# Performance work log

Hardware: AMD Instinct MI355X
Metric: run time of the kernel (lower is better)

Reference implementation:

```python
import jax, jax.numpy as jnp
import numpy as np

B, DIM, N = 4, 256, 2048
HEADS, DIM_HEAD = 8, 64
HIDDEN = HEADS * DIM_HEAD
SCALE = DIM_HEAD ** -0.5


def setup_inputs() -> dict:
    key = jax.random.key(0)
    k0, k1, k2, k3 = jax.random.split(key, 4)
    x = jax.random.normal(k0, (B, DIM, N), dtype=jnp.float32)
    # Conv1d kernel-size-1 weights == plain matrices over channels
    w_qkv = jax.random.normal(k1, (3 * HIDDEN, DIM), dtype=jnp.float32) * (DIM ** -0.5)
    w_out = jax.random.normal(k2, (DIM, HIDDEN), dtype=jnp.float32) * (HIDDEN ** -0.5)
    b_out = jax.random.normal(k3, (DIM,), dtype=jnp.float32) * 0.01
    return {"x": x, "w_qkv": w_qkv, "w_out": w_out, "b_out": b_out}


def reference(x, w_qkv, w_out, b_out):
    b, c, n = x.shape
    # 1x1 conv projection: [3H, C] x [b, C, n] -> [b, 3H, n]
    qkv = jnp.einsum('oc,bcn->bon', w_qkv, x)
    q, k, v = jnp.split(qkv, 3, axis=1)
    # [b, heads, dim_head, n]
    q = q.reshape(b, HEADS, DIM_HEAD, n) * SCALE
    k = k.reshape(b, HEADS, DIM_HEAD, n)
    v = v.reshape(b, HEADS, DIM_HEAD, n)
    sim = jnp.einsum('bhcn,bhcm->bhnm', q, k)          # [b,h,n,n]
    attn = jax.nn.softmax(sim, axis=-1)
    out = jnp.einsum('bhnm,bhcm->bhcn', attn, v)       # [b,h,dh,n]
    out = out.reshape(b, HIDDEN, n)
    return jnp.einsum('oc,bcn->bon', w_out, out) + b_out[None, :, None]
```

## Files before the change

### kernel.cpp

```cpp
#include <hip/hip_runtime.h>
#include <math.h>

#define BB 4
#define CDIM 256
#define NN 2048
#define HEADS 8
#define DH 64
#define HIDDEN 512
#define THREEH 1536
#define QSCALE 0.18033688011112042f

typedef __attribute__((ext_vector_type(8))) short bf16x8;
typedef __attribute__((ext_vector_type(4))) float f32x4;
typedef __attribute__((ext_vector_type(4))) unsigned uint4v;

static __device__ inline unsigned short f2bf(float f) {
    unsigned u = __float_as_uint(f);
    u += 0x7fff + ((u >> 16) & 1);
    return (unsigned short)(u >> 16);
}
#if __has_builtin(__builtin_amdgcn_cvt_pk_bf16_f32)
static __device__ inline unsigned pk2(float a, float b) {
    auto v = __builtin_amdgcn_cvt_pk_bf16_f32(a, b);
    return __builtin_bit_cast(unsigned, v);
}
#else
static __device__ inline unsigned pk2(float a, float b) {
    return (unsigned)f2bf(a) | ((unsigned)f2bf(b) << 16);
}
#endif
#if __has_builtin(__builtin_amdgcn_exp2f)
#define EXP2(x) __builtin_amdgcn_exp2f(x)
#else
#define EXP2(x) exp2f(x)
#endif
#define MFMA16(a, b, c) __builtin_amdgcn_mfma_f32_16x16x32_bf16(a, b, c, 0, 0, 0)
#define SWZC(row, ch) ((((ch) ^ ((row) & 7)) << 3))

static __device__ inline void swap16(unsigned &a, unsigned &b) {
    asm("v_permlane16_swap_b32 %0, %1" : "+v"(a), "+v"(b));
}
static __device__ inline void swap32(unsigned &a, unsigned &b) {
    asm("v_permlane32_swap_b32 %0, %1" : "+v"(a), "+v"(b));
}

__global__ __launch_bounds__(256) void prep_all(const float* __restrict__ x,
                                                const float* __restrict__ wqkv,
                                                const float* __restrict__ wout,
                                                unsigned short* __restrict__ Xt,
                                                unsigned* __restrict__ Wqb,
                                                unsigned* __restrict__ Wob) {
    __shared__ float Ls[64][65];
    const int bx = blockIdx.x;
    if (bx < 512) {
        const int n0 = (bx & 31) * 64, c0 = ((bx >> 5) & 3) * 64, b = bx >> 7;
        const int t = threadIdx.x;
        const int r16 = t >> 4, c16 = t & 15;
#pragma unroll
        for (int s = 0; s < 4; ++s) {
            const int c = s * 16 + r16;
            float4 v = *(const float4*)&x[((size_t)(b * CDIM + c0 + c)) * NN + n0 + c16 * 4];
            *(float4*)&Ls[c][c16 * 4] = v;
        }
        __syncthreads();
#pragma unroll
        for (int s = 0; s < 4; ++s) {
            const int n = s * 16 + r16;
            const int c4 = c16 * 4;
            uint2 u;
            u.x = pk2(Ls[c4][n], Ls[c4 + 1][n]);
            u.y = pk2(Ls[c4 + 2][n], Ls[c4 + 3][n]);
            *(uint2*)&Xt[((size_t)(b * NN) + n0 + n) * CDIM + c0 + c4] = u;
        }
    } else if (bx < 536) {
        const int tt = (bx - 512) * 256 + threadIdx.x;
#pragma unroll 4
        for (int j = 0; j < 16; ++j) {
            const int i4 = tt + j * 6144;
            const int e = i4 * 4;
            const float s = ((e >> 8) < HIDDEN) ? QSCALE : 1.f;
            float4 v = *(const float4*)&wqkv[e];
            Wqb[i4 * 2 + 0] = pk2(v.x * s, v.y * s);
            Wqb[i4 * 2 + 1] = pk2(v.z * s, v.w * s);
        }
    } else {
        const int tt = (bx - 536) * 256 + threadIdx.x;
#pragma unroll 4
        for (int j = 0; j < 16; ++j) {
            const int i4 = tt + j * 2048;
            const int e = i4 * 4;
            float4 v = *(const float4*)&wout[e];
            Wob[i4 * 2 + 0] = pk2(v.x, v.y);
            Wob[i4 * 2 + 1] = pk2(v.z, v.w);
        }
    }
}

__global__ __launch_bounds__(256, 3) void qkv_gemm(const unsigned short* __restrict__ Xt,
                                                   const unsigned short* __restrict__ Wqb,
                                                   unsigned short* __restrict__ Qb,
                                                   unsigned short* __restrict__ Kb,
                                                   unsigned short* __restrict__ Vb) {
    __shared__ unsigned short Xs[128 * 64], Ws[128 * 64];
    const int bn0 = blockIdx.x * 128, o0 = blockIdx.y * 128;
    const int t = threadIdx.x, l = t & 63, w = t >> 6, lo = l & 15, quad = l >> 4;
    const int wo = (w >> 1) * 64, wn = (w & 1) * 64;
    const int sr = t >> 1, scb = (t & 1) * 4;
    const bool isV = (o0 >= 2 * HIDDEN);
    f32x4 acc[4][4];
#pragma unroll
    for (int i = 0; i < 4; ++i)
#pragma unroll
        for (int j = 0; j < 4; ++j) acc[i][j] = (f32x4){0.f, 0.f, 0.f, 0.f};

    for (int kc = 0; kc < CDIM; kc += 64) {
        __syncthreads();
#pragma unroll
        for (int j = 0; j < 4; ++j) {
            const int ch = scb + j;
            *(uint4*)&Xs[sr * 64 + SWZC(sr, ch)] =
                *(const uint4*)&Xt[(size_t)(bn0 + sr) * CDIM + kc + ch * 8];
            *(uint4*)&Ws[sr * 64 + SWZC(sr, ch)] =
                *(const uint4*)&Wqb[(size_t)(o0 + sr) * CDIM + kc + ch * 8];
        }
        __syncthreads();
#pragma unroll
        for (int kk = 0; kk < 2; ++kk) {
            const int swz = SWZC(lo, kk * 4 + quad);
            if (!isV) {
                bf16x8 af[4], bv[4];
#pragma unroll
                for (int ot = 0; ot < 4; ++ot) af[ot] = *(const bf16x8*)&Ws[(wo + ot * 16 + lo) * 64 + swz];
#pragma unroll
                for (int nt = 0; nt < 4; ++nt) bv[nt] = *(const bf16x8*)&Xs[(wn + nt * 16 + lo) * 64 + swz];
#pragma unroll
                for (int ot = 0; ot < 4; ++ot)
#pragma unroll
                    for (int nt = 0; nt < 4; ++nt) acc[ot][nt] = MFMA16(af[ot], bv[nt], acc[ot][nt]);
            } else {
                bf16x8 af[4], bv[4];
#pragma unroll
                for (int mt = 0; mt < 4; ++mt) af[mt] = *(const bf16x8*)&Xs[(wn + mt * 16 + lo) * 64 + swz];
#pragma unroll
                for (int ot = 0; ot < 4; ++ot) bv[ot] = *(const bf16x8*)&Ws[(wo + ot * 16 + lo) * 64 + swz];
#pragma unroll
                for (int mt = 0; mt < 4; ++mt)
#pragma unroll
                    for (int ot = 0; ot < 4; ++ot) acc[mt][ot] = MFMA16(af[mt], bv[ot], acc[mt][ot]);
            }
        }
    }
    if (!isV) {
#pragma unroll
        for (int ot = 0; ot < 4; ++ot) {
            const int og = o0 + wo + ot * 16 + quad * 4;
            const int h = (og >> 6) & 7;
            const int c0 = og & 63;
            unsigned short* dst = (og >= HIDDEN) ? Kb : Qb;
#pragma unroll
            for (int nt = 0; nt < 4; ++nt) {
                const int bn = bn0 + wn + nt * 16 + lo;
                const int b = bn >> 11, n = bn & 2047;
                uint2 u;
                u.x = pk2(acc[ot][nt][0], acc[ot][nt][1]);
                u.y = pk2(acc[ot][nt][2], acc[ot][nt][3]);
                *(uint2*)&dst[(((size_t)(b * HEADS + h)) * NN + n) * DH + c0] = u;
            }
        }
    } else {
#pragma unroll
        for (int mt = 0; mt < 4; ++mt) {
            const int bn = bn0 + wn + mt * 16 + quad * 4;
            const int b = bn >> 11, m = bn & 2047;
#pragma unroll
            for (int ot = 0; ot < 4; ++ot) {
                const int og = o0 + wo + ot * 16 + lo;
                const int h = (og >> 6) & 7;
                const int c = og & 63;
                uint2 u;
                u.x = pk2(acc[mt][ot][0], acc[mt][ot][1]);
                u.y = pk2(acc[mt][ot][2], acc[mt][ot][3]);
                *(uint2*)&Vb[(((size_t)(b * HEADS + h)) * DH + c) * NN + m] = u;
            }
        }
    }
}

__global__ __launch_bounds__(256, 4) void flash_attn(const unsigned short* __restrict__ Qb,
                                                     const unsigned short* __restrict__ Kb,
                                                     const unsigned short* __restrict__ Vb,
                                                     unsigned short* __restrict__ Yb) {
    __shared__ unsigned short Ks[64 * 64], Vs[64 * 64];
    const int flat = blockIdx.x;
    const int rest = flat >> 3;
    const int bh = ((rest & 3) << 3) | (flat & 7);
    const int q0 = (rest >> 2) * 128;
    const int b = bh >> 3, h = bh & 7;
    const int t = threadIdx.x, l = t & 63, w = t >> 6, lo = l & 15, quad = l >> 4;
    const unsigned short* Qp = Qb + (size_t)bh * NN * DH;
    const unsigned short* Kp = Kb + (size_t)bh * NN * DH;
    const unsigned short* Vp = Vb + (size_t)bh * DH * NN;
    const int qbase = q0 + 32 * w;
    bf16x8 bQ[2][2];
#pragma unroll
    for (int qt = 0; qt < 2; ++qt)
#pragma unroll
        for (int hh = 0; hh < 2; ++hh)
            bQ[qt][hh] = *(const bf16x8*)&Qp[(size_t)(qbase + qt * 16 + lo) * DH + hh * 32 + quad * 8];
    f32x4 O[4][2], lacc[2];
#pragma unroll
    for (int i = 0; i < 4; ++i)
#pragma unroll
        for (int j = 0; j < 2; ++j) O[i][j] = (f32x4){0.f, 0.f, 0.f, 0.f};
#pragma unroll
    for (int j = 0; j < 2; ++j) lacc[j] = (f32x4){0.f, 0.f, 0.f, 0.f};
    bf16x8 aOnes;
    {
        const short v = (lo == 0) ? (short)0x3F80 : (short)0;
        aOnes = (bf16x8){v, v, v, v, v, v, v, v};
    }
    const int sr = t >> 3, sc = t & 7;
    const int kst0 = sr * 64 + SWZC(sr, sc);
    uint4 rk0 = *(const uint4*)&Kp[(size_t)sr * DH + sc * 8];
    uint4 rk1 = *(const uint4*)&Kp[(size_t)(sr + 32) * DH + sc * 8];
    uint4 rv0 = *(const uint4*)&Vp[(size_t)sr * NN + sc * 8];
    uint4 rv1 = *(const uint4*)&Vp[(size_t)(sr + 32) * NN + sc * 8];

#pragma unroll 1
    for (int m0 = 0; m0 < NN; m0 += 64) {
        __syncthreads();
        *(uint4*)&Ks[kst0] = rk0;
        *(uint4*)&Ks[kst0 + 2048] = rk1;
        *(uint4*)&Vs[kst0] = rv0;
        *(uint4*)&Vs[kst0 + 2048] = rv1;
        __syncthreads();
        {
            const int m1 = (m0 + 64 < NN) ? (m0 + 64) : m0;
            rk0 = *(const uint4*)&Kp[(size_t)(m1 + sr) * DH + sc * 8];
            rk1 = *(const uint4*)&Kp[(size_t)(m1 + sr + 32) * DH + sc * 8];
            rv0 = *(const uint4*)&Vp[(size_t)sr * NN + m1 + sc * 8];
            rv1 = *(const uint4*)&Vp[(size_t)(sr + 32) * NN + m1 + sc * 8];
        }
        unsigned wv[2][4][2];
#pragma unroll
        for (int nt = 0; nt < 4; ++nt) {
            const int rb = (nt * 16 + lo) * 64;
            bf16x8 a0 = *(const bf16x8*)&Ks[rb + SWZC(lo, quad)];
            bf16x8 a1 = *(const bf16x8*)&Ks[rb + SWZC(lo, quad + 4)];
#pragma unroll
            for (int qt = 0; qt < 2; ++qt) {
                f32x4 z = (f32x4){0.f, 0.f, 0.f, 0.f};
                z = MFMA16(a0, bQ[qt][0], z);
                z = MFMA16(a1, bQ[qt][1], z);
                wv[qt][nt][0] = pk2(EXP2(z[0]), EXP2(z[1]));
                wv[qt][nt][1] = pk2(EXP2(z[2]), EXP2(z[3]));
            }
        }
        bf16x8 pb[2][2];
#pragma unroll
        for (int qt = 0; qt < 2; ++qt) {
#pragma unroll
            for (int f = 0; f < 2; ++f) {
                unsigned x0 = wv[qt][2 * f][0], y0 = wv[qt][2 * f + 1][0];
                unsigned x1 = wv[qt][2 * f][1], y1 = wv[qt][2 * f + 1][1];
                swap32(x0, y0); swap16(x0, y0);
                swap32(x1, y1); swap16(x1, y1);
                uint4v uu;
                uu.x = x0; uu.y = x1; uu.z = y0; uu.w = y1;
                pb[qt][f] = __builtin_bit_cast(bf16x8, uu);
            }
        }
#pragma unroll
        for (int ct = 0; ct < 4; ++ct) {
            const int rb = (ct * 16 + lo) * 64;
            bf16x8 a0 = *(const bf16x8*)&Vs[rb + SWZC(lo, quad)];
            bf16x8 a1 = *(const bf16x8*)&Vs[rb + SWZC(lo, quad + 4)];
            __builtin_amdgcn_s_setprio(1);
#pragma unroll
            for (int qt = 0; qt < 2; ++qt) {
                O[ct][qt] = MFMA16(a0, pb[qt][0], O[ct][qt]);
                O[ct][qt] = MFMA16(a1, pb[qt][1], O[ct][qt]);
            }
            __builtin_amdgcn_s_setprio(0);
        }
#pragma unroll
        for (int qt = 0; qt < 2; ++qt) {
            lacc[qt] = MFMA16(aOnes, pb[qt][0], lacc[qt]);
            lacc[qt] = MFMA16(aOnes, pb[qt][1], lacc[qt]);
        }
    }
#pragma unroll
    for (int qt = 0; qt < 2; ++qt) {
        const float lv = __shfl(lacc[qt][0], lo);
        const float inv = 1.f / lv;
        const int q = qbase + qt * 16 + lo;
        unsigned short* yrow = Yb + ((size_t)(b * NN) + q) * HIDDEN + h * DH;
#pragma unroll
        for (int ct = 0; ct < 4; ++ct) {
            uint2 u;
            u.x = pk2(O[ct][qt][0] * inv, O[ct][qt][1] * inv);
            u.y = pk2(O[ct][qt][2] * inv, O[ct][qt][3] * inv);
            *(uint2*)&yrow[ct * 16 + quad * 4] = u;
        }
    }
}

__global__ __launch_bounds__(256, 4) void out_gemm(const unsigned short* __restrict__ Yb,
                                                   const unsigned short* __restrict__ Wob,
                                                   const float* __restrict__ bias,
                                                   float* __restrict__ out) {
    __shared__ unsigned short Ys[128 * 64], Wos[64 * 64];
    const int bn0 = blockIdx.x * 128, o0 = blockIdx.y * 64;
    const int t = threadIdx.x, l = t & 63, w = t >> 6, lo = l & 15, quad = l >> 4;
    const int wn = w * 32;
    const int sr = t >> 1, scb = (t & 1) * 4;
    const int sr2 = t >> 2, scb2 = (t & 3) * 2;
    f32x4 acc[2][4];
#pragma unroll
    for (int i = 0; i < 2; ++i)
#pragma unroll
        for (int j = 0; j < 4; ++j) acc[i][j] = (f32x4){0.f, 0.f, 0.f, 0.f};

    for (int kc = 0; kc < HIDDEN; kc += 64) {
        __syncthreads();
#pragma unroll
        for (int j = 0; j < 4; ++j) {
            const int ch = scb + j;
            *(uint4*)&Ys[sr * 64 + SWZC(sr, ch)] =
                *(const uint4*)&Yb[(size_t)(bn0 + sr) * HIDDEN + kc + ch * 8];
        }
#pragma unroll
        for (int j = 0; j < 2; ++j) {
            const int ch = scb2 + j;
            *(uint4*)&Wos[sr2 * 64 + SWZC(sr2, ch)] =
                *(const uint4*)&Wob[(size_t)(o0 + sr2) * HIDDEN + kc + ch * 8];
        }
        __syncthreads();
#pragma unroll
        for (int kk = 0; kk < 2; ++kk) {
            const int swz = SWZC(lo, kk * 4 + quad);
            bf16x8 bv[4];
#pragma unroll
            for (int ot = 0; ot < 4; ++ot) bv[ot] = *(const bf16x8*)&Wos[(ot * 16 + lo) * 64 + swz];
#pragma unroll
            for (int mt = 0; mt < 2; ++mt) {
                bf16x8 av = *(const bf16x8*)&Ys[(wn + mt * 16 + lo) * 64 + swz];
#pragma unroll
                for (int ot = 0; ot < 4; ++ot) acc[mt][ot] = MFMA16(av, bv[ot], acc[mt][ot]);
            }
        }
    }
#pragma unroll
    for (int mt = 0; mt < 2; ++mt) {
        const int bn = bn0 + wn + mt * 16 + quad * 4;
        const int b = bn >> 11, n = bn & 2047;
#pragma unroll
        for (int ot = 0; ot < 4; ++ot) {
            const int o = o0 + ot * 16 + lo;
            *(f32x4*)&out[((size_t)(b * CDIM + o)) * NN + n] = acc[mt][ot] + bias[o];
        }
    }
}

extern "C" void kernel_launch(void* const* d_in, const int* in_sizes, int n_in,
                              void* d_out, int out_size, void* d_ws, size_t ws_size,
                              hipStream_t stream) {
    const float* x     = (const float*)d_in[0];
    const float* w_qkv = (const float*)d_in[1];
    const float* w_out = (const float*)d_in[2];
    const float* b_out = (const float*)d_in[3];
    float* out = (float*)d_out;

    unsigned short* Wqb = (unsigned short*)d_ws;
    unsigned short* Wob = Wqb + (size_t)THREEH * CDIM;
    unsigned short* Xt  = Wob + (size_t)CDIM * HIDDEN;
    unsigned short* Qb  = Xt + (size_t)BB * NN * CDIM;
    unsigned short* Kb  = Qb + (size_t)BB * HEADS * NN * DH;
    unsigned short* Vb  = Kb + (size_t)BB * HEADS * NN * DH;
    unsigned short* Yb  = Vb + (size_t)BB * HEADS * DH * NN;

    prep_all<<<544, 256, 0, stream>>>(x, w_qkv, w_out, Xt, (unsigned*)Wqb, (unsigned*)Wob);
    qkv_gemm<<<dim3(BB * NN / 128, THREEH / 128), 256, 0, stream>>>(Xt, Wqb, Qb, Kb, Vb);
    flash_attn<<<512, 256, 0, stream>>>(Qb, Kb, Vb, Yb);
    out_gemm<<<dim3(BB * NN / 128, CDIM / 64), 256, 0, stream>>>(Yb, Wob, b_out, out);
}
```

Baseline: 148.4 us.

## Load K/V MFMA fragments directly from global memory with register double-buffering

The flash attention kernel no longer stages K and V tiles through shared memory with two barriers per tile. Each wave now loads its MFMA operand fragments straight from global memory into registers, ping-ponging between two register sets and prefetching the next tile while the current one is computed. The goal is to remove LDS traffic and block-wide synchronisation. In exchange, each of the 4 waves fetches the full K/V tile itself (4x redundant global/L2 reads), register use rises, and occupancy is lowered to 2 blocks per CU.

```diff
diff --git a/kernel.cpp b/kernel.cpp
--- a/kernel.cpp
+++ b/kernel.cpp
@@ -186,11 +186,71 @@
     }
 }
 
-__global__ __launch_bounds__(256, 4) void flash_attn(const unsigned short* __restrict__ Qb,
+#define LOADK(D0, D1, m)                                                       \
+    {                                                                          \
+        _Pragma("unroll")                                                      \
+        for (int nt = 0; nt < 4; ++nt) {                                       \
+            D0[nt] = *(const bf16x8*)&kRow[(size_t)((m) + nt * 16) * DH];      \
+            D1[nt] = *(const bf16x8*)&kRow[(size_t)((m) + nt * 16) * DH + 32]; \
+        }                                                                      \
+    }
+#define LOADV(D0, D1, m)                                                       \
+    {                                                                          \
+        _Pragma("unroll")                                                      \
+        for (int ct = 0; ct < 4; ++ct) {                                       \
+            D0[ct] = *(const bf16x8*)&vRow[(size_t)(ct * 16) * NN + (m)];      \
+            D1[ct] = *(const bf16x8*)&vRow[(size_t)(ct * 16) * NN + (m) + 32]; \
+        }                                                                      \
+    }
+#define TILE(K0, K1, V0, V1)                                                   \
+    {                                                                          \
+        unsigned wv[2][4][2];                                                  \
+        _Pragma("unroll")                                                      \
+        for (int nt = 0; nt < 4; ++nt) {                                       \
+            _Pragma("unroll")                                                  \
+            for (int qt = 0; qt < 2; ++qt) {                                   \
+                f32x4 z = (f32x4){0.f, 0.f, 0.f, 0.f};                         \
+                z = MFMA16(K0[nt], bQ[qt][0], z);                              \
+                z = MFMA16(K1[nt], bQ[qt][1], z);                              \
+                wv[qt][nt][0] = pk2(EXP2(z[0]), EXP2(z[1]));                   \
+                wv[qt][nt][1] = pk2(EXP2(z[2]), EXP2(z[3]));                   \
+            }                                                                  \
+        }                                                                      \
+        bf16x8 pb[2][2];                                                       \
+        _Pragma("unroll")                                                      \
+        for (int qt = 0; qt < 2; ++qt) {                                       \
+            _Pragma("unroll")                                                  \
+            for (int f = 0; f < 2; ++f) {                                      \
+                unsigned x0 = wv[qt][2 * f][0], y0 = wv[qt][2 * f + 1][0];     \
+                unsigned x1 = wv[qt][2 * f][1], y1 = wv[qt][2 * f + 1][1];     \
+                swap32(x0, y0); swap16(x0, y0);                                \
+                swap32(x1, y1); swap16(x1, y1);                                \
+                uint4v uu;                                                     \
+                uu.x = x0; uu.y = x1; uu.z = y0; uu.w = y1;                    \
+                pb[qt][f] = __builtin_bit_cast(bf16x8, uu);                    \
+            }                                                                  \
+        }                                                                      \
+        __builtin_amdgcn_s_setprio(1);                                         \
+        _Pragma("unroll")                                                      \
+        for (int ct = 0; ct < 4; ++ct) {                                       \
+            _Pragma("unroll")                                                  \
+            for (int qt = 0; qt < 2; ++qt) {                                   \
+                O[ct][qt] = MFMA16(V0[ct], pb[qt][0], O[ct][qt]);              \
+                O[ct][qt] = MFMA16(V1[ct], pb[qt][1], O[ct][qt]);              \
+            }                                                                  \
+        }                                                                      \
+        __builtin_amdgcn_s_setprio(0);                                         \
+        _Pragma("unroll")                                                      \
+        for (int qt = 0; qt < 2; ++qt) {                                       \
+            lacc[qt] = MFMA16(aOnes, pb[qt][0], lacc[qt]);                     \
+            lacc[qt] = MFMA16(aOnes, pb[qt][1], lacc[qt]);                     \
+        }                                                                      \
+    }
+
+__global__ __launch_bounds__(256, 2) void flash_attn(const unsigned short* __restrict__ Qb,
                                                      const unsigned short* __restrict__ Kb,
                                                      const unsigned short* __restrict__ Vb,
                                                      unsigned short* __restrict__ Yb) {
-    __shared__ unsigned short Ks[64 * 64], Vs[64 * 64];
     const int flat = blockIdx.x;
     const int rest = flat >> 3;
     const int bh = ((rest & 3) << 3) | (flat & 7);
@@ -219,75 +279,22 @@
         const short v = (lo == 0) ? (short)0x3F80 : (short)0;
         aOnes = (bf16x8){v, v, v, v, v, v, v, v};
     }
-    const int sr = t >> 3, sc = t & 7;
-    const int kst0 = sr * 64 + SWZC(sr, sc);
-    uint4 rk0 = *(const uint4*)&Kp[(size_t)sr * DH + sc * 8];
-    uint4 rk1 = *(const uint4*)&Kp[(size_t)(sr + 32) * DH + sc * 8];
-    uint4 rv0 = *(const uint4*)&Vp[(size_t)sr * NN + sc * 8];
-    uint4 rv1 = *(const uint4*)&Vp[(size_t)(sr + 32) * NN + sc * 8];
-
+    const unsigned short* kRow = Kp + (size_t)lo * DH + quad * 8;
+    const unsigned short* vRow = Vp + (size_t)lo * NN + quad * 8;
+
+    bf16x8 kA0[4], kA1[4], kB0[4], kB1[4], vA0[4], vA1[4], vB0[4], vB1[4];
+    LOADK(kA0, kA1, 0);
 #pragma unroll 1
-    for (int m0 = 0; m0 < NN; m0 += 64) {
-        __syncthreads();
-        *(uint4*)&Ks[kst0] = rk0;
-        *(uint4*)&Ks[kst0 + 2048] = rk1;
-        *(uint4*)&Vs[kst0] = rv0;
-        *(uint4*)&Vs[kst0 + 2048] = rv1;
-        __syncthreads();
+    for (int m0 = 0; m0 < NN; m0 += 128) {
+        LOADV(vA0, vA1, m0);
+        LOADK(kB0, kB1, m0 + 64);
+        TILE(kA0, kA1, vA0, vA1);
+        LOADV(vB0, vB1, m0 + 64);
         {
-            const int m1 = (m0 + 64 < NN) ? (m0 + 64) : m0;
-            rk0 = *(const uint4*)&Kp[(size_t)(m1 + sr) * DH + sc * 8];
-            rk1 = *(const uint4*)&Kp[(size_t)(m1 + sr + 32) * DH + sc * 8];
-            rv0 = *(const uint4*)&Vp[(size_t)sr * NN + m1 + sc * 8];
-            rv1 = *(const uint4*)&Vp[(size_t)(sr + 32) * NN + m1 + sc * 8];
-        }
-        unsigned wv[2][4][2];
-#pragma unroll
-        for (int nt = 0; nt < 4; ++nt) {
-            const int rb = (nt * 16 + lo) * 64;
-            bf16x8 a0 = *(const bf16x8*)&Ks[rb + SWZC(lo, quad)];
-            bf16x8 a1 = *(const bf16x8*)&Ks[rb + SWZC(lo, quad + 4)];
-#pragma unroll
-            for (int qt = 0; qt < 2; ++qt) {
-                f32x4 z = (f32x4){0.f, 0.f, 0.f, 0.f};
-                z = MFMA16(a0, bQ[qt][0], z);
-                z = MFMA16(a1, bQ[qt][1], z);
-                wv[qt][nt][0] = pk2(EXP2(z[0]), EXP2(z[1]));
-                wv[qt][nt][1] = pk2(EXP2(z[2]), EXP2(z[3]));
-            }
-        }
-        bf16x8 pb[2][2];
-#pragma unroll
-        for (int qt = 0; qt < 2; ++qt) {
-#pragma unroll
-            for (int f = 0; f < 2; ++f) {
-                unsigned x0 = wv[qt][2 * f][0], y0 = wv[qt][2 * f + 1][0];
-                unsigned x1 = wv[qt][2 * f][1], y1 = wv[qt][2 * f + 1][1];
-                swap32(x0, y0); swap16(x0, y0);
-                swap32(x1, y1); swap16(x1, y1);
-                uint4v uu;
-                uu.x = x0; uu.y = x1; uu.z = y0; uu.w = y1;
-                pb[qt][f] = __builtin_bit_cast(bf16x8, uu);
-            }
-        }
-#pragma unroll
-        for (int ct = 0; ct < 4; ++ct) {
-            const int rb = (ct * 16 + lo) * 64;
-            bf16x8 a0 = *(const bf16x8*)&Vs[rb + SWZC(lo, quad)];
-            bf16x8 a1 = *(const bf16x8*)&Vs[rb + SWZC(lo, quad + 4)];
-            __builtin_amdgcn_s_setprio(1);
-#pragma unroll
-            for (int qt = 0; qt < 2; ++qt) {
-                O[ct][qt] = MFMA16(a0, pb[qt][0], O[ct][qt]);
-                O[ct][qt] = MFMA16(a1, pb[qt][1], O[ct][qt]);
-            }
-            __builtin_amdgcn_s_setprio(0);
-        }
-#pragma unroll
-        for (int qt = 0; qt < 2; ++qt) {
-            lacc[qt] = MFMA16(aOnes, pb[qt][0], lacc[qt]);
-            lacc[qt] = MFMA16(aOnes, pb[qt][1], lacc[qt]);
-        }
+            const int mn = (m0 + 128 < NN) ? (m0 + 128) : 0;
+            LOADK(kA0, kA1, mn);
+        }
+        TILE(kB0, kB1, vB0, vB1);
     }
 #pragma unroll
     for (int qt = 0; qt < 2; ++qt) {
```

New measurement: 216.8 us. +46.1%, slower.
